# Kernel tuning notes

Hardware: AMD Instinct MI355X
Metric: run time of the kernel (lower is better)

Reference implementation:

```python
import jax, jax.numpy as jnp
import numpy as np

D_MODEL = 1024
NUM_HEADS = 16
THETA = 10000.0


def _rope_tables(seq_len, d_k, dtype):
    # k = 1..d_k/2, freq = theta**(-(2k-2)/d_k)
    k = jnp.arange(1, d_k // 2 + 1, dtype=jnp.float32)
    freq = 1.0 / THETA ** ((2.0 * k - 2.0) / d_k)
    pos = jnp.arange(seq_len, dtype=jnp.float32)
    ang = pos[:, None] * freq[None, :]  # [S, d_k/2]
    return jnp.cos(ang).astype(dtype), jnp.sin(ang).astype(dtype)


def _apply_rope(x, cos, sin):
    # x: [..., S, d_k]; pairs are interleaved (even, odd)
    xe = x[..., 0::2]
    xo = x[..., 1::2]
    rot_e = xe * cos - xo * sin
    rot_o = xe * sin + xo * cos
    # interleave back: (d (1+1))
    out = jnp.stack([rot_e, rot_o], axis=-1)
    return out.reshape(x.shape)


def setup_inputs() -> dict:
    key = jax.random.key(0)
    ks = jax.random.split(key, 5)
    B, S, D = 2, 2048, D_MODEL
    std = np.sqrt(2.0 / (D + D))
    x = jax.random.normal(ks[0], (B, S, D), dtype=jnp.float32)
    Wq = jax.random.truncated_normal(ks[1], -3.0, 3.0, (D, D), dtype=jnp.float32) * std
    Wk = jax.random.truncated_normal(ks[2], -3.0, 3.0, (D, D), dtype=jnp.float32) * std
    Wv = jax.random.truncated_normal(ks[3], -3.0, 3.0, (D, D), dtype=jnp.float32) * std
    Wo = jax.random.truncated_normal(ks[4], -3.0, 3.0, (D, D), dtype=jnp.float32) * std
    return {"x": x, "Wq": Wq, "Wk": Wk, "Wv": Wv, "Wo": Wo}


def reference(x, Wq, Wk, Wv, Wo):
    B, S, D = x.shape
    h = NUM_HEADS
    dk = D // h

    def split_heads(t):
        return t.reshape(B, S, h, dk).transpose(0, 2, 1, 3)  # [B, h, S, dk]

    Q = split_heads(jnp.einsum('bsd,od->bso', x, Wq))
    K = split_heads(jnp.einsum('bsd,od->bso', x, Wk))
    V = split_heads(jnp.einsum('bsd,od->bso', x, Wv))

    cos, sin = _rope_tables(S, dk, x.dtype)
    Q = _apply_rope(Q, cos, sin)
    K = _apply_rope(K, cos, sin)

    scores = jnp.einsum('bhqd,bhkd->bhqk', Q, K) / jnp.sqrt(jnp.asarray(dk, x.dtype))
    causal = jnp.tril(jnp.ones((S, S), dtype=bool))
    scores = jnp.where(causal, scores, -jnp.inf)
    attn = jax.nn.softmax(scores, axis=-1)
    out = jnp.einsum('bhqk,bhkd->bhqd', attn, V)  # [B, h, S, dk]
    out = out.transpose(0, 2, 1, 3).reshape(B, S, D)
    return jnp.einsum('bsd,od->bso', out, Wo)
```

## Files before the change

kernel.cpp:

```cpp
#include <hip/hip_runtime.h>
#include <hip/hip_fp16.h>

#define BATCH 2
#define D_MODEL 1024
#define NH 16
#define DK 64
#define SEQ 2048

typedef _Float16 f16;
typedef __attribute__((ext_vector_type(8))) _Float16 f16x8;
typedef __attribute__((ext_vector_type(4))) _Float16 f16x4;
typedef __attribute__((ext_vector_type(4))) float f32x4;

__global__ __launch_bounds__(256) void gemm_qkv(const float* __restrict__ X,
                                                const float* __restrict__ Wq,
                                                const float* __restrict__ Wk,
                                                const float* __restrict__ Wv,
                                                f16* __restrict__ WS)
{
    constexpr int BK  = 32;
    constexpr int LDP = BK + 8;
    __shared__ f16 As[128 * LDP];
    __shared__ f16 Bs[128 * LDP];

    const int tid  = threadIdx.x;
    const int lane = tid & 63;
    const int wave = tid >> 6;
    const int wm   = wave >> 1, wn = wave & 1;
    const int m0   = blockIdx.y * 128;
    const int n0   = blockIdx.x * 128;
    const int seg  = n0 >> 10;
    const int nloc = n0 & 1023;
    const float* __restrict__ W = (seg == 0) ? Wq : (seg == 1 ? Wk : Wv);
    const int do_rope = (seg < 2);
    f16* __restrict__ Out = WS + (size_t)seg * BATCH * SEQ * D_MODEL;

    f32x4 acc[4][4] = {};

    const int srow = tid >> 3;
    const int scol = (tid & 7) * 4;

    for (int k0 = 0; k0 < 1024; k0 += BK) {
        __syncthreads();
        #pragma unroll
        for (int p = 0; p < 4; ++p) {
            int r = p * 32 + srow;
            float4 v = *(const float4*)(X + (size_t)(m0 + r) * 1024 + k0 + scol);
            f16x4 h; h[0]=(f16)v.x; h[1]=(f16)v.y; h[2]=(f16)v.z; h[3]=(f16)v.w;
            *(f16x4*)(As + r * LDP + scol) = h;
            float4 w = *(const float4*)(W + (size_t)(nloc + r) * 1024 + k0 + scol);
            f16x4 hw; hw[0]=(f16)w.x; hw[1]=(f16)w.y; hw[2]=(f16)w.z; hw[3]=(f16)w.w;
            *(f16x4*)(Bs + r * LDP + scol) = hw;
        }
        __syncthreads();

        const int kc = (lane >> 4) * 8;
        f16x8 a[4], b[4];
        #pragma unroll
        for (int i = 0; i < 4; ++i) {
            a[i] = *(const f16x8*)(As + (wm*64 + i*16 + (lane & 15)) * LDP + kc);
            b[i] = *(const f16x8*)(Bs + (wn*64 + i*16 + (lane & 15)) * LDP + kc);
        }
        #pragma unroll
        for (int i = 0; i < 4; ++i)
            #pragma unroll
            for (int j = 0; j < 4; ++j)
                acc[i][j] = __builtin_amdgcn_mfma_f32_16x16x32_f16(a[i], b[j], acc[i][j], 0, 0, 0);
    }

    const int rbase = m0 + wm * 64 + ((lane >> 4) * 4);
    const int cbase = nloc + wn * 64 + (lane & 15);
    #pragma unroll
    for (int j = 0; j < 4; ++j) {
        const int o  = cbase + j * 16;
        const int hh = o >> 6;
        const int d  = o & 63;
        const float freq = do_rope ? powf(10000.f, -(float)(d >> 1) * (1.f / 32.f)) : 0.f;
        #pragma unroll
        for (int i = 0; i < 4; ++i) {
            #pragma unroll
            for (int r = 0; r < 4; ++r) {
                const int row = rbase + i * 16 + r;
                const int b   = row >> 11;
                const int s   = row & 2047;
                float v    = acc[i][j][r];
                float outv = v;
                float partner = __shfl_xor(v, 1);
                if (do_rope) {
                    float ang = (float)s * freq;
                    float sn, cs;
                    sincosf(ang, &sn, &cs);
                    outv = (d & 1) ? (partner * sn + v * cs) : (v * cs - partner * sn);
                }
                Out[((size_t)(b * NH + hh) * SEQ + s) * DK + d] = (f16)outv;
            }
        }
    }
}

__global__ __launch_bounds__(256) void attn(const f16* __restrict__ Q,
                                            const f16* __restrict__ K,
                                            const f16* __restrict__ V,
                                            f16* __restrict__ O)
{
    constexpr int SP = 72;
    __shared__ f16 Kt[64 * SP];
    __shared__ f16 Vt[64 * SP];
    __shared__ f16 Pt[64 * SP];

    const int tid  = threadIdx.x;
    const int lane = tid & 63;
    const int w    = tid >> 6;
    const int g    = lane >> 4;
    const int l15  = lane & 15;
    const int qb = blockIdx.x, hh = blockIdx.y, b = blockIdx.z;
    const int q0 = qb * 64;
    const size_t base = (size_t)(b * NH + hh) * SEQ * DK;

    f16x8 qf[2];
    {
        const f16* qp = Q + base + (size_t)(q0 + w * 16 + l15) * DK + g * 8;
        qf[0] = *(const f16x8*)(qp);
        qf[1] = *(const f16x8*)(qp + 32);
    }
    f32x4 acc[4] = {};
    float m_reg[4] = {-INFINITY, -INFINITY, -INFINITY, -INFINITY};
    float l_reg[4] = {0.f, 0.f, 0.f, 0.f};

    for (int kb = 0; kb <= qb; ++kb) {
        __syncthreads();
        {
            #pragma unroll
            for (int it = 0; it < 2; ++it) {
                const int c  = tid + it * 256;
                const int kk = c >> 3;
                const int dc = (c & 7) * 8;
                f16x8 kv = *(const f16x8*)(K + base + (size_t)(kb * 64 + kk) * DK + dc);
                *(f16x8*)(Kt + kk * SP + dc) = kv;
                f16x8 vv = *(const f16x8*)(V + base + (size_t)(kb * 64 + kk) * DK + dc);
                const int swz = ((dc >> 3) & 3) << 3;
                #pragma unroll
                for (int e = 0; e < 8; ++e)
                    Vt[(dc + e) * SP + (kk ^ swz)] = vv[e];
            }
        }
        __syncthreads();

        f32x4 s[4];
        #pragma unroll
        for (int nt = 0; nt < 4; ++nt) {
            f32x4 z = {};
            const f16* kp = Kt + (nt * 16 + l15) * SP + g * 8;
            z = __builtin_amdgcn_mfma_f32_16x16x32_f16(qf[0], *(const f16x8*)kp,        z, 0, 0, 0);
            z = __builtin_amdgcn_mfma_f32_16x16x32_f16(qf[1], *(const f16x8*)(kp + 32), z, 0, 0, 0);
            s[nt] = z;
        }

        #pragma unroll
        for (int r = 0; r < 4; ++r) {
            const int qloc = w * 16 + g * 4 + r;
            float va[4];
            #pragma unroll
            for (int nt = 0; nt < 4; ++nt) {
                float sv = s[nt][r] * 0.125f;
                if (kb == qb && (nt * 16 + l15) > qloc) sv = -INFINITY;
                va[nt] = sv;
            }
            float mx = fmaxf(fmaxf(va[0], va[1]), fmaxf(va[2], va[3]));
            mx = fmaxf(mx, __shfl_xor(mx, 1));
            mx = fmaxf(mx, __shfl_xor(mx, 2));
            mx = fmaxf(mx, __shfl_xor(mx, 4));
            mx = fmaxf(mx, __shfl_xor(mx, 8));
            const float mnew = fmaxf(m_reg[r], mx);
            const float scl  = __expf(m_reg[r] - mnew);
            m_reg[r] = mnew;
            float ps = 0.f;
            #pragma unroll
            for (int nt = 0; nt < 4; ++nt) {
                float p = __expf(va[nt] - mnew);
                ps += p;
                Pt[qloc * SP + nt * 16 + l15] = (f16)p;
            }
            ps += __shfl_xor(ps, 1);
            ps += __shfl_xor(ps, 2);
            ps += __shfl_xor(ps, 4);
            ps += __shfl_xor(ps, 8);
            l_reg[r] = l_reg[r] * scl + ps;
            #pragma unroll
            for (int nt = 0; nt < 4; ++nt) acc[nt][r] *= scl;
        }

        {
            f16x8 pa[2];
            const f16* pp = Pt + (w * 16 + l15) * SP + g * 8;
            pa[0] = *(const f16x8*)pp;
            pa[1] = *(const f16x8*)(pp + 32);
            #pragma unroll
            for (int nt = 0; nt < 4; ++nt) {
                const int d = nt * 16 + l15;
                const int m = ((d >> 3) & 3);
                const int c0 = ((g ^ m) << 3);
                const f16* vp = Vt + d * SP;
                f16x8 vb0 = *(const f16x8*)(vp + c0);
                f16x8 vb1 = *(const f16x8*)(vp + c0 + 32);
                acc[nt] = __builtin_amdgcn_mfma_f32_16x16x32_f16(pa[0], vb0, acc[nt], 0, 0, 0);
                acc[nt] = __builtin_amdgcn_mfma_f32_16x16x32_f16(pa[1], vb1, acc[nt], 0, 0, 0);
            }
        }
    }

    #pragma unroll
    for (int r = 0; r < 4; ++r) {
        const float inv = 1.f / l_reg[r];
        const int s = q0 + w * 16 + g * 4 + r;
        #pragma unroll
        for (int nt = 0; nt < 4; ++nt) {
            const int d = nt * 16 + l15;
            O[((size_t)(b * SEQ + s)) * D_MODEL + hh * 64 + d] = (f16)(acc[nt][r] * inv);
        }
    }
}

__global__ __launch_bounds__(256) void gemm_out(const f16* __restrict__ A,
                                                const float* __restrict__ W,
                                                float* __restrict__ Cout)
{
    constexpr int BK  = 32;
    constexpr int LDP = BK + 8;
    __shared__ f16 As[64 * LDP];
    __shared__ f16 Bs[128 * LDP];

    const int tid  = threadIdx.x;
    const int lane = tid & 63;
    const int wave = tid >> 6;
    const int wm   = wave >> 1, wn = wave & 1;
    const int m0   = blockIdx.y * 64;
    const int n0   = blockIdx.x * 128;

    f32x4 acc[2][4] = {};

    const int srow = tid >> 3;
    const int scol = (tid & 7) * 4;
    const int arow = tid >> 2;
    const int acol = (tid & 3) * 8;

    for (int k0 = 0; k0 < 1024; k0 += BK) {
        __syncthreads();
        {
            f16x8 v = *(const f16x8*)(A + (size_t)(m0 + arow) * 1024 + k0 + acol);
            *(f16x8*)(As + arow * LDP + acol) = v;
        }
        #pragma unroll
        for (int p = 0; p < 4; ++p) {
            int r = p * 32 + srow;
            float4 w = *(const float4*)(W + (size_t)(n0 + r) * 1024 + k0 + scol);
            f16x4 hw; hw[0]=(f16)w.x; hw[1]=(f16)w.y; hw[2]=(f16)w.z; hw[3]=(f16)w.w;
            *(f16x4*)(Bs + r * LDP + scol) = hw;
        }
        __syncthreads();

        const int kc = (lane >> 4) * 8;
        f16x8 a[2], b[4];
        #pragma unroll
        for (int i = 0; i < 2; ++i)
            a[i] = *(const f16x8*)(As + (wm*32 + i*16 + (lane & 15)) * LDP + kc);
        #pragma unroll
        for (int j = 0; j < 4; ++j)
            b[j] = *(const f16x8*)(Bs + (wn*64 + j*16 + (lane & 15)) * LDP + kc);
        #pragma unroll
        for (int i = 0; i < 2; ++i)
            #pragma unroll
            for (int j = 0; j < 4; ++j)
                acc[i][j] = __builtin_amdgcn_mfma_f32_16x16x32_f16(a[i], b[j], acc[i][j], 0, 0, 0);
    }

    #pragma unroll
    for (int i = 0; i < 2; ++i)
        #pragma unroll
        for (int j = 0; j < 4; ++j)
            #pragma unroll
            for (int r = 0; r < 4; ++r) {
                const int row = m0 + wm*32 + i*16 + ((lane >> 4) * 4) + r;
                const int col = n0 + wn*64 + j*16 + (lane & 15);
                Cout[(size_t)row * 1024 + col] = acc[i][j][r];
            }
}

extern "C" void kernel_launch(void* const* d_in, const int* in_sizes, int n_in,
                              void* d_out, int out_size, void* d_ws, size_t ws_size,
                              hipStream_t stream)
{
    const float* x  = (const float*)d_in[0];
    const float* Wq = (const float*)d_in[1];
    const float* Wk = (const float*)d_in[2];
    const float* Wv = (const float*)d_in[3];
    const float* Wo = (const float*)d_in[4];
    float* out = (float*)d_out;

    const size_t NE = (size_t)BATCH * SEQ * D_MODEL;
    f16* Qr = (f16*)d_ws;
    f16* Kr = Qr + NE;
    f16* Vr = Kr + NE;
    f16* AO = Vr + NE;

    dim3 blk(256);
    gemm_qkv<<<dim3(24, 32), blk, 0, stream>>>(x, Wq, Wk, Wv, Qr);

    attn<<<dim3(SEQ / 64, NH, BATCH), blk, 0, stream>>>(Qr, Kr, Vr, AO);

    gemm_out<<<dim3(8, 64), blk, 0, stream>>>(AO, Wo, out);
}
```

Baseline: 370.0 us.

## Store V pre-transposed from QKV GEMM and schedule heavy causal blocks first

The QKV projection now writes V in a [b,h,d,s] transposed layout, so the attention kernel can load V tiles with vectorized 16-byte copies instead of scattered per-element transposing stores into shared memory. The V-operand read in the PV MFMA loses its swizzle logic. Attention blocks are issued in reverse query-block order so the longest causal rows start first, which should reduce tail imbalance. The transposed V stores in the GEMM epilogue are strided (one element per SEQ stride), which may cost some write efficiency there. The RoPE branch is also split out so the V path skips the shuffle.

Measured after the change: 787.6 us. 113% more time.

```diff
diff --git a/kernel.cpp b/kernel.cpp
--- a/kernel.cpp
+++ b/kernel.cpp
@@ -32,7 +32,6 @@
     const int seg  = n0 >> 10;
     const int nloc = n0 & 1023;
     const float* __restrict__ W = (seg == 0) ? Wq : (seg == 1 ? Wk : Wv);
-    const int do_rope = (seg < 2);
     f16* __restrict__ Out = WS + (size_t)seg * BATCH * SEQ * D_MODEL;
 
     f32x4 acc[4][4] = {};
@@ -70,29 +69,45 @@
 
     const int rbase = m0 + wm * 64 + ((lane >> 4) * 4);
     const int cbase = nloc + wn * 64 + (lane & 15);
-    #pragma unroll
-    for (int j = 0; j < 4; ++j) {
-        const int o  = cbase + j * 16;
-        const int hh = o >> 6;
-        const int d  = o & 63;
-        const float freq = do_rope ? powf(10000.f, -(float)(d >> 1) * (1.f / 32.f)) : 0.f;
-        #pragma unroll
-        for (int i = 0; i < 4; ++i) {
-            #pragma unroll
-            for (int r = 0; r < 4; ++r) {
-                const int row = rbase + i * 16 + r;
-                const int b   = row >> 11;
-                const int s   = row & 2047;
-                float v    = acc[i][j][r];
-                float outv = v;
-                float partner = __shfl_xor(v, 1);
-                if (do_rope) {
+    if (seg < 2) {
+        #pragma unroll
+        for (int j = 0; j < 4; ++j) {
+            const int o  = cbase + j * 16;
+            const int hh = o >> 6;
+            const int d  = o & 63;
+            const float freq = powf(10000.f, -(float)(d >> 1) * (1.f / 32.f));
+            #pragma unroll
+            for (int i = 0; i < 4; ++i) {
+                #pragma unroll
+                for (int r = 0; r < 4; ++r) {
+                    const int row = rbase + i * 16 + r;
+                    const int b   = row >> 11;
+                    const int s   = row & 2047;
+                    float v = acc[i][j][r];
+                    float partner = __shfl_xor(v, 1);
                     float ang = (float)s * freq;
                     float sn, cs;
                     sincosf(ang, &sn, &cs);
-                    outv = (d & 1) ? (partner * sn + v * cs) : (v * cs - partner * sn);
+                    float outv = (d & 1) ? (partner * sn + v * cs) : (v * cs - partner * sn);
+                    Out[((size_t)(b * NH + hh) * SEQ + s) * DK + d] = (f16)outv;
                 }
-                Out[((size_t)(b * NH + hh) * SEQ + s) * DK + d] = (f16)outv;
+            }
+        }
+    } else {
+        #pragma unroll
+        for (int j = 0; j < 4; ++j) {
+            const int o  = cbase + j * 16;
+            const int hh = o >> 6;
+            const int d  = o & 63;
+            #pragma unroll
+            for (int i = 0; i < 4; ++i) {
+                #pragma unroll
+                for (int r = 0; r < 4; ++r) {
+                    const int row = rbase + i * 16 + r;
+                    const int b   = row >> 11;
+                    const int s   = row & 2047;
+                    Out[((size_t)(b * NH + hh) * DK + d) * SEQ + s] = (f16)acc[i][j][r];
+                }
             }
         }
     }
@@ -100,7 +115,7 @@
 
 __global__ __launch_bounds__(256) void attn(const f16* __restrict__ Q,
                                             const f16* __restrict__ K,
-                                            const f16* __restrict__ V,
+                                            const f16* __restrict__ VT,
                                             f16* __restrict__ O)
 {
     constexpr int SP = 72;
@@ -113,7 +128,8 @@
     const int w    = tid >> 6;
     const int g    = lane >> 4;
     const int l15  = lane & 15;
-    const int qb = blockIdx.x, hh = blockIdx.y, b = blockIdx.z;
+    const int qb = gridDim.x - 1 - blockIdx.x;
+    const int hh = blockIdx.y, b = blockIdx.z;
     const int q0 = qb * 64;
     const size_t base = (size_t)(b * NH + hh) * SEQ * DK;
 
@@ -127,21 +143,19 @@
     float m_reg[4] = {-INFINITY, -INFINITY, -INFINITY, -INFINITY};
     float l_reg[4] = {0.f, 0.f, 0.f, 0.f};
 
+    const int srow = tid >> 3;
+    const int sco  = (tid & 7) * 8;
+
     for (int kb = 0; kb <= qb; ++kb) {
         __syncthreads();
         {
             #pragma unroll
             for (int it = 0; it < 2; ++it) {
-                const int c  = tid + it * 256;
-                const int kk = c >> 3;
-                const int dc = (c & 7) * 8;
-                f16x8 kv = *(const f16x8*)(K + base + (size_t)(kb * 64 + kk) * DK + dc);
-                *(f16x8*)(Kt + kk * SP + dc) = kv;
-                f16x8 vv = *(const f16x8*)(V + base + (size_t)(kb * 64 + kk) * DK + dc);
-                const int swz = ((dc >> 3) & 3) << 3;
-                #pragma unroll
-                for (int e = 0; e < 8; ++e)
-                    Vt[(dc + e) * SP + (kk ^ swz)] = vv[e];
+                const int rr = it * 32 + srow;
+                f16x8 kv = *(const f16x8*)(K + base + (size_t)(kb * 64 + rr) * DK + sco);
+                *(f16x8*)(Kt + rr * SP + sco) = kv;
+                f16x8 vv = *(const f16x8*)(VT + base + (size_t)rr * SEQ + kb * 64 + sco);
+                *(f16x8*)(Vt + rr * SP + sco) = vv;
             }
         }
         __syncthreads();
@@ -197,14 +211,9 @@
             pa[1] = *(const f16x8*)(pp + 32);
             #pragma unroll
             for (int nt = 0; nt < 4; ++nt) {
-                const int d = nt * 16 + l15;
-                const int m = ((d >> 3) & 3);
-                const int c0 = ((g ^ m) << 3);
-                const f16* vp = Vt + d * SP;
-                f16x8 vb0 = *(const f16x8*)(vp + c0);
-                f16x8 vb1 = *(const f16x8*)(vp + c0 + 32);
-                acc[nt] = __builtin_amdgcn_mfma_f32_16x16x32_f16(pa[0], vb0, acc[nt], 0, 0, 0);
-                acc[nt] = __builtin_amdgcn_mfma_f32_16x16x32_f16(pa[1], vb1, acc[nt], 0, 0, 0);
+                const f16* vp = Vt + (nt * 16 + l15) * SP + g * 8;
+                acc[nt] = __builtin_amdgcn_mfma_f32_16x16x32_f16(pa[0], *(const f16x8*)vp,        acc[nt], 0, 0, 0);
+                acc[nt] = __builtin_amdgcn_mfma_f32_16x16x32_f16(pa[1], *(const f16x8*)(vp + 32), acc[nt], 0, 0, 0);
             }
         }
     }
@@ -300,13 +309,13 @@
     const size_t NE = (size_t)BATCH * SEQ * D_MODEL;
     f16* Qr = (f16*)d_ws;
     f16* Kr = Qr + NE;
-    f16* Vr = Kr + NE;
-    f16* AO = Vr + NE;
+    f16* VTr = Kr + NE;
+    f16* AO = VTr + NE;
 
     dim3 blk(256);
     gemm_qkv<<<dim3(24, 32), blk, 0, stream>>>(x, Wq, Wk, Wv, Qr);
 
-    attn<<<dim3(SEQ / 64, NH, BATCH), blk, 0, stream>>>(Qr, Kr, Vr, AO);
+    attn<<<dim3(SEQ / 64, NH, BATCH), blk, 0, stream>>>(Qr, Kr, VTr, AO);
 
     gemm_out<<<dim3(8, 64), blk, 0, stream>>>(AO, Wo, out);
 }
```
